# Optimization experiments

Hardware: AMD Instinct MI355X
Metric: run time of the kernel (lower is better)

The kernel has to match this reference:

```python
import jax, jax.numpy as jnp
import numpy as np

HIDDEN = 1024
HEADS = 16
HEAD_DIM = HIDDEN // HEADS


def setup_inputs() -> dict:
    key = jax.random.key(0)
    kx, kw = jax.random.split(key)
    x = jax.random.normal(kx, (1, 4096, HIDDEN), dtype=jnp.float32)
    # torch Linear weight is [out, in]; we store as [in, out] for x @ W
    W_qkv = jax.random.normal(kw, (HIDDEN, 3 * HIDDEN), dtype=jnp.float32) * (HIDDEN ** -0.5)
    return {"x": x, "W_qkv": W_qkv}


def reference(x, W_qkv):
    B, T, _ = x.shape
    qkv = x @ W_qkv                                    # [B, T, 3*HIDDEN]
    qkv = qkv.reshape(B, T, 3, HEADS, HEAD_DIM)
    qkv = jnp.transpose(qkv, (2, 0, 3, 1, 4))          # [3, B, H, T, Dh]
    q, k, v = qkv[0], qkv[1], qkv[2]
    scale = HEAD_DIM ** -0.5
    attn = jnp.einsum("bhqd,bhkd->bhqk", q, k) * scale  # [B, H, T, T] materialized (naive)
    attn = jax.nn.softmax(attn, axis=-1)
    out = jnp.einsum("bhqk,bhkd->bhqd", attn, v)        # [B, H, T, Dh]
    out = jnp.transpose(out, (0, 2, 1, 3)).reshape(B, T, HIDDEN)
    return out
```

## Files before the change

kernel.cpp:

```cpp
#include <hip/hip_runtime.h>

#define SEQ 4096
#define HID 1024
#define NH  16
#define DH  64
#define N3  3072

typedef __attribute__((ext_vector_type(4))) float floatx4;
typedef __attribute__((ext_vector_type(8))) short shortx8;
typedef __attribute__((ext_vector_type(4))) short shortx4;

__device__ __forceinline__ short f2bf(float f) {
    return (short)((__builtin_bit_cast(unsigned, f) + 0x8000u) >> 16);
}
__device__ __forceinline__ unsigned pk2bf(float a, float b) {
    unsigned ua = __builtin_bit_cast(unsigned, a) + 0x8000u;
    unsigned ub = __builtin_bit_cast(unsigned, b) + 0x8000u;
    return (ua >> 16) | (ub & 0xFFFF0000u);
}
__device__ __forceinline__ shortx4 pk4bf(float a, float b, float c, float d) {
    union { unsigned u[2]; shortx4 s; } x;
    x.u[0] = pk2bf(a, b);
    x.u[1] = pk2bf(c, d);
    return x.s;
}

#if __has_builtin(__builtin_amdgcn_exp2f)
#define fexp2 __builtin_amdgcn_exp2f
#else
#define fexp2 exp2f
#endif

#define mfma32 __builtin_amdgcn_mfma_f32_16x16x32_bf16

__device__ __forceinline__ void gll16(const short* g, short* l) {
    __builtin_amdgcn_global_load_lds(
        (const __attribute__((address_space(1))) unsigned*)g,
        (__attribute__((address_space(3))) unsigned*)l, 16, 0, 0);
}

__global__ __launch_bounds__(256) void convert_x(
    const float* __restrict__ x, short* __restrict__ Xb)
{
    size_t i = (size_t)blockIdx.x * 256 + threadIdx.x;
    float4 v = *(const float4*)&x[i * 4];
    shortx4 b = pk4bf(v.x, v.y, v.z, v.w);
    *(shortx4*)&Xb[i * 4] = b;
}

__global__ __launch_bounds__(256) void transpose_W(
    const float* __restrict__ W, short* __restrict__ Wt)
{
    __shared__ short Ws[128 * 40];
    const int t  = threadIdx.x;
    const int n0 = blockIdx.x * 128;
    const int k0 = blockIdx.y * 32;
    #pragma unroll
    for (int i = 0; i < 4; i++) {
        int idx = t + i * 256;
        int k = idx >> 5, c4 = idx & 31;
        float4 v = *(const float4*)&W[(size_t)(k0 + k) * N3 + n0 + c4 * 4];
        Ws[(c4 * 4 + 0) * 40 + k] = f2bf(v.x);
        Ws[(c4 * 4 + 1) * 40 + k] = f2bf(v.y);
        Ws[(c4 * 4 + 2) * 40 + k] = f2bf(v.z);
        Ws[(c4 * 4 + 3) * 40 + k] = f2bf(v.w);
    }
    __syncthreads();
    #pragma unroll
    for (int i = 0; i < 2; i++) {
        int idx = t + i * 256;
        int n = idx >> 2, seg = idx & 3;
        shortx8 g = *(const shortx8*)&Ws[n * 40 + seg * 8];
        *(shortx8*)&Wt[(size_t)(n0 + n) * HID + k0 + seg * 8] = g;
    }
}

#define LDC 136
__global__ __launch_bounds__(256) void qkv_gemm(
    const short* __restrict__ Xb, const short* __restrict__ Wt,
    short* __restrict__ Qb, short* __restrict__ Kb, short* __restrict__ Vb)
{
    __shared__ short SM[18432];
    short* As = SM;
    short* Bs = SM + 128 * 64;
    const int tid  = threadIdx.x;
    const int m0   = blockIdx.x * 128;
    const int n0   = blockIdx.y * 128;
    const int lane = tid & 63;
    const int wid  = tid >> 6;
    const int wm   = (wid >> 1) * 64;
    const int wn   = (wid & 1) * 64;
    const int l15  = lane & 15;
    const int quad = lane >> 4;

    floatx4 acc[4][4];
    #pragma unroll
    for (int i = 0; i < 4; i++)
        #pragma unroll
        for (int j = 0; j < 4; j++)
            acc[i][j] = (floatx4){0.f, 0.f, 0.f, 0.f};

    const int arow = tid >> 3, ac = tid & 7;
    const int swk  = (ac ^ (arow & 7)) << 3;
    const short* ag = Xb + (size_t)(m0 + arow) * HID + swk;
    const short* bg = Wt + (size_t)(n0 + arow) * HID + swk;
    short* al = As + (size_t)(tid & 192) * 8;
    short* bl = Bs + (size_t)(tid & 192) * 8;
    const int r7 = l15 & 7;

    for (int k0 = 0; k0 < HID; k0 += 64) {
        #pragma unroll
        for (int i = 0; i < 4; i++)
            gll16(ag + (size_t)i * 32 * HID + k0, al + i * 2048);
        #pragma unroll
        for (int i = 0; i < 4; i++)
            gll16(bg + (size_t)i * 32 * HID + k0, bl + i * 2048);
        __syncthreads();
        #pragma unroll
        for (int kh = 0; kh < 2; kh++) {
            shortx8 af[4], bf[4];
            #pragma unroll
            for (int t = 0; t < 4; t++) {
                int R = wm + t * 16 + l15;
                af[t] = *(const shortx8*)&As[(R << 6) + ((((kh << 2) + quad) ^ r7) << 3)];
                int Rb = wn + t * 16 + l15;
                bf[t] = *(const shortx8*)&Bs[(Rb << 6) + ((((kh << 2) + quad) ^ r7) << 3)];
            }
            #pragma unroll
            for (int tm = 0; tm < 4; tm++)
                #pragma unroll
                for (int tn = 0; tn < 4; tn++)
                    acc[tm][tn] = mfma32(af[tm], bf[tn], acc[tm][tn], 0, 0, 0);
        }
        __syncthreads();
    }

    short* Cs = SM;
    const float sc = (n0 < 1024) ? 0.18033688011112042f : 1.0f;
    #pragma unroll
    for (int tm = 0; tm < 4; tm++)
        #pragma unroll
        for (int tn = 0; tn < 4; tn++)
            #pragma unroll
            for (int r = 0; r < 4; r++)
                Cs[(wm + tm * 16 + quad * 4 + r) * LDC + wn + tn * 16 + l15] =
                    f2bf(acc[tm][tn][r] * sc);
    __syncthreads();
    short* base = (n0 < 1024) ? Qb : (n0 < 2048 ? Kb : Vb);
    const int h0 = (n0 & 1023) >> 6;
    #pragma unroll
    for (int j = 0; j < 8; j++) {
        int idx = tid + j * 256;
        int row = idx >> 4, col = (idx & 15) * 8;
        shortx8 v = *(const shortx8*)&Cs[row * LDC + col];
        *(shortx8*)&base[((size_t)(h0 + (col >> 6)) * SEQ + m0 + row) * DH + (col & 63)] = v;
    }
}

__global__ __launch_bounds__(256) void transpose_V(
    const short* __restrict__ Vb, short* __restrict__ Vt)
{
    __shared__ short Ts[64 * 72];
    const int t  = threadIdx.x;
    const int t0 = blockIdx.x * 64;
    const int h  = blockIdx.y;
    #pragma unroll
    for (int i = 0; i < 2; i++) {
        int idx = t + i * 256;
        int r = idx >> 3, seg = idx & 7;
        shortx8 g = *(const shortx8*)&Vb[((size_t)h * SEQ + t0 + r) * DH + seg * 8];
        *(shortx8*)&Ts[r * 72 + seg * 8] = g;
    }
    __syncthreads();
    #pragma unroll
    for (int i = 0; i < 2; i++) {
        int idx = t + i * 256;
        int d = idx >> 3, tseg = idx & 7;
        shortx8 g;
        #pragma unroll
        for (int j = 0; j < 8; j++) g[j] = Ts[(tseg * 8 + j) * 72 + d];
        *(shortx8*)&Vt[((size_t)h * DH + d) * SEQ + t0 + tseg * 8] = g;
    }
}

__global__ __launch_bounds__(256) void flash_attn(
    const short* __restrict__ Qb, const short* __restrict__ Kb,
    const short* __restrict__ Vt, float* __restrict__ out,
    float* __restrict__ Opart, float* __restrict__ Lpart,
    int kpc, int nit, int final)
{
    __shared__ short Ks[2][4096];
    __shared__ short Vs[2][4096];
    const int tid  = threadIdx.x;
    const int lane = tid & 63;
    const int l15  = lane & 15;
    const int quad = lane >> 4;
    const int h    = blockIdx.y;
    const int ch   = blockIdx.z;
    const int q0   = blockIdx.x * 128 + (tid >> 6) * 32;
    const int tstart = ch * kpc;
    const shortx8 ones8 = {(short)0x3F80, (short)0x3F80, (short)0x3F80, (short)0x3F80,
                           (short)0x3F80, (short)0x3F80, (short)0x3F80, (short)0x3F80};

    const short* qp = Qb + ((size_t)h * SEQ + q0 + l15) * DH;
    shortx8 qf00 = *(const shortx8*)(qp + quad * 8);
    shortx8 qf01 = *(const shortx8*)(qp + 32 + quad * 8);
    shortx8 qf10 = *(const shortx8*)(qp + 16 * DH + quad * 8);
    shortx8 qf11 = *(const shortx8*)(qp + 16 * DH + 32 + quad * 8);

    floatx4 oacc[2][4];
    #pragma unroll
    for (int s = 0; s < 2; s++)
        #pragma unroll
        for (int dn = 0; dn < 4; dn++)
            oacc[s][dn] = (floatx4){0.f, 0.f, 0.f, 0.f};
    floatx4 lacc0 = {0.f, 0.f, 0.f, 0.f}, lacc1 = {0.f, 0.f, 0.f, 0.f};

    const int rK   = tid >> 3, sK = tid & 7;
    const int key0 = 8 * ((rK >> 2) & 3) + 4 * ((rK >> 4) & 1) + (rK & 3);
    const int swo  = (sK ^ (rK & 7)) << 3;
    const short* kg = Kb + ((size_t)h * SEQ + tstart + key0) * DH + swo;
    const short* vg = Vt + ((size_t)h * DH + rK) * SEQ + tstart + swo;
    const int wslot = (tid & 192) * 8;

    gll16(kg,            &Ks[0][wslot]);
    gll16(kg + 32 * DH,  &Ks[0][wslot + 2048]);
    gll16(vg,            &Vs[0][wslot]);
    gll16(vg + 32 * SEQ, &Vs[0][wslot + 2048]);
    kg += 64 * DH;  vg += 64;

    for (int it = 0; it < nit; it++) {
        __syncthreads();
        if (it + 1 < nit) {
            int b = (it + 1) & 1;
            gll16(kg,            &Ks[b][wslot]);
            gll16(kg + 32 * DH,  &Ks[b][wslot + 2048]);
            gll16(vg,            &Vs[b][wslot]);
            gll16(vg + 32 * SEQ, &Vs[b][wslot + 2048]);
            kg += 64 * DH;  vg += 64;
        }
        const short* ks = Ks[it & 1];
        const short* vs = Vs[it & 1];

        floatx4 st0[4], st1[4];
        #pragma unroll
        for (int tn = 0; tn < 4; tn++) {
            int R = tn * 16 + l15;
            int off = (R << 6) + ((quad ^ (R & 7)) << 3);
            shortx8 kf0 = *(const shortx8*)&ks[off];
            shortx8 kf1 = *(const shortx8*)&ks[off ^ 32];
            floatx4 a0 = {0.f, 0.f, 0.f, 0.f};
            a0 = mfma32(kf0, qf00, a0, 0, 0, 0);
            a0 = mfma32(kf1, qf01, a0, 0, 0, 0);
            st0[tn] = a0;
            floatx4 a1 = {0.f, 0.f, 0.f, 0.f};
            a1 = mfma32(kf0, qf10, a1, 0, 0, 0);
            a1 = mfma32(kf1, qf11, a1, 0, 0, 0);
            st1[tn] = a1;
        }

        union { unsigned u[4]; shortx8 s; } pa00, pa01, pa10, pa11;
        #pragma unroll
        for (int half = 0; half < 2; half++) {
            int ta = half * 2, tb = half * 2 + 1;
            unsigned* d0 = half ? pa01.u : pa00.u;
            unsigned* d1 = half ? pa11.u : pa10.u;
            d0[0] = pk2bf(fexp2(st0[ta][0]), fexp2(st0[ta][1]));
            d0[1] = pk2bf(fexp2(st0[ta][2]), fexp2(st0[ta][3]));
            d0[2] = pk2bf(fexp2(st0[tb][0]), fexp2(st0[tb][1]));
            d0[3] = pk2bf(fexp2(st0[tb][2]), fexp2(st0[tb][3]));
            d1[0] = pk2bf(fexp2(st1[ta][0]), fexp2(st1[ta][1]));
            d1[1] = pk2bf(fexp2(st1[ta][2]), fexp2(st1[ta][3]));
            d1[2] = pk2bf(fexp2(st1[tb][0]), fexp2(st1[tb][1]));
            d1[3] = pk2bf(fexp2(st1[tb][2]), fexp2(st1[tb][3]));
        }

        lacc0 = mfma32(pa00.s, ones8, lacc0, 0, 0, 0);
        lacc0 = mfma32(pa01.s, ones8, lacc0, 0, 0, 0);
        lacc1 = mfma32(pa10.s, ones8, lacc1, 0, 0, 0);
        lacc1 = mfma32(pa11.s, ones8, lacc1, 0, 0, 0);

        #pragma unroll
        for (int dn = 0; dn < 4; dn++) {
            int row = dn * 16 + l15;
            int off = (row << 6) + ((quad ^ (row & 7)) << 3);
            shortx8 va = *(const shortx8*)&vs[off];
            shortx8 vb = *(const shortx8*)&vs[off ^ 32];
            oacc[0][dn] = mfma32(pa00.s, va, oacc[0][dn], 0, 0, 0);
            oacc[0][dn] = mfma32(pa01.s, vb, oacc[0][dn], 0, 0, 0);
            oacc[1][dn] = mfma32(pa10.s, va, oacc[1][dn], 0, 0, 0);
            oacc[1][dn] = mfma32(pa11.s, vb, oacc[1][dn], 0, 0, 0);
        }
    }

    if (final) {
        #pragma unroll
        for (int r = 0; r < 4; r++) {
            float rl0 = 1.0f / lacc0[r], rl1 = 1.0f / lacc1[r];
            int query = q0 + quad * 4 + r;
            float* d0 = out + (size_t)query * HID + h * DH + l15;
            float* d1 = d0 + (size_t)16 * HID;
            #pragma unroll
            for (int dn = 0; dn < 4; dn++) {
                d0[dn * 16] = oacc[0][dn][r] * rl0;
                d1[dn * 16] = oacc[1][dn][r] * rl1;
            }
        }
    } else {
        #pragma unroll
        for (int r = 0; r < 4; r++) {
            int query = q0 + quad * 4 + r;
            float* d0 = Opart + ((size_t)ch * SEQ + query) * HID + h * DH + l15;
            float* d1 = d0 + (size_t)16 * HID;
            #pragma unroll
            for (int dn = 0; dn < 4; dn++) {
                d0[dn * 16] = oacc[0][dn][r];
                d1[dn * 16] = oacc[1][dn][r];
            }
        }
        if (l15 == 0) {
            float* lp = Lpart + ((size_t)ch * NH + h) * SEQ + q0;
            #pragma unroll
            for (int r = 0; r < 4; r++) {
                lp[quad * 4 + r]      = lacc0[r];
                lp[16 + quad * 4 + r] = lacc1[r];
            }
        }
    }
}

__global__ __launch_bounds__(256) void combine(
    const float* __restrict__ Opart, const float* __restrict__ Lpart,
    float* __restrict__ out, int chn)
{
    size_t i = ((size_t)blockIdx.x * 256 + threadIdx.x) * 4;
    int q = (int)(i >> 10);
    int h = ((int)i & 1023) >> 6;
    float4 o = {0.f, 0.f, 0.f, 0.f};
    float l = 0.f;
    for (int c = 0; c < chn; c++) {
        float4 p = *(const float4*)&Opart[(size_t)c * SEQ * HID + i];
        o.x += p.x; o.y += p.y; o.z += p.z; o.w += p.w;
        l += Lpart[((size_t)c * NH + h) * SEQ + q];
    }
    float rl = 1.0f / l;
    float4 r = {o.x * rl, o.y * rl, o.z * rl, o.w * rl};
    *(float4*)&out[i] = r;
}

extern "C" void kernel_launch(void* const* d_in, const int* in_sizes, int n_in,
                              void* d_out, int out_size, void* d_ws, size_t ws_size,
                              hipStream_t stream) {
    const float* x = (const float*)d_in[0];
    const float* W = (const float*)d_in[1];
    float* out = (float*)d_out;

    short* Xb = (short*)d_ws;
    short* Wt = Xb + (size_t)SEQ * HID;
    short* Qb = Wt + (size_t)N3 * HID;
    short* Kb = Qb + (size_t)NH * SEQ * DH;
    short* Vb = Kb + (size_t)NH * SEQ * DH;
    short* Vt = Xb;
    float* Opart = (float*)(Vb + (size_t)NH * SEQ * DH);

    const size_t need = 39845888ull
                      + 4ull * SEQ * HID * 4
                      + 4ull * NH * SEQ * 4;
    const int chn = (ws_size >= need) ? 4 : 1;
    float* Lpart = Opart + (size_t)chn * SEQ * HID;
    const int kpc = SEQ / chn, nit = kpc / 64;

    convert_x  <<<dim3(SEQ * HID / 1024), 256, 0, stream>>>(x, Xb);
    transpose_W<<<dim3(N3 / 128, HID / 32), 256, 0, stream>>>(W, Wt);
    qkv_gemm   <<<dim3(SEQ / 128, N3 / 128), 256, 0, stream>>>(Xb, Wt, Qb, Kb, Vb);
    transpose_V<<<dim3(SEQ / 64, NH), 256, 0, stream>>>(Vb, Vt);
    flash_attn <<<dim3(SEQ / 128, NH, chn), 256, 0, stream>>>(
        Qb, Kb, Vt, out, Opart, Lpart, kpc, nit, chn == 1);
    if (chn > 1)
        combine<<<dim3(SEQ * HID / 1024), 256, 0, stream>>>(Opart, Lpart, out, chn);
}
```

Before: 214.5 us.

## Software-pipeline flash attention PV with next QK and swap GEMM grid order

The flash attention loop is restructured so the P·V MFMAs for the previous tile run while the current tile's QK scores are computed, and the exp/pack work is deferred. V gets a triple buffer so the tile still being consumed is not overwritten by the prefetch. A prologue and epilogue handle the first and last tiles. Separately, the QKV GEMM grid is transposed so consecutive blocks walk along N, which changes L2 reuse of the X and W tiles. The cost is more shared memory and more live registers in the attention kernel.

Measured after the change: 216.4 us. No clear change (+0.9%).

```diff
diff --git a/kernel.cpp b/kernel.cpp
--- a/kernel.cpp
+++ b/kernel.cpp
@@ -84,8 +84,8 @@
     short* As = SM;
     short* Bs = SM + 128 * 64;
     const int tid  = threadIdx.x;
-    const int m0   = blockIdx.x * 128;
-    const int n0   = blockIdx.y * 128;
+    const int n0   = blockIdx.x * 128;
+    const int m0   = blockIdx.y * 128;
     const int lane = tid & 63;
     const int wid  = tid >> 6;
     const int wm   = (wid >> 1) * 64;
@@ -190,7 +190,7 @@
     int kpc, int nit, int final)
 {
     __shared__ short Ks[2][4096];
-    __shared__ short Vs[2][4096];
+    __shared__ short Vs[3][4096];
     const int tid  = threadIdx.x;
     const int lane = tid & 63;
     const int l15  = lane & 15;
@@ -228,19 +228,67 @@
     gll16(vg,            &Vs[0][wslot]);
     gll16(vg + 32 * SEQ, &Vs[0][wslot + 2048]);
     kg += 64 * DH;  vg += 64;
-
-    for (int it = 0; it < nit; it++) {
+    __syncthreads();
+    if (nit > 1) {
+        gll16(kg,            &Ks[1][wslot]);
+        gll16(kg + 32 * DH,  &Ks[1][wslot + 2048]);
+        gll16(vg,            &Vs[1][wslot]);
+        gll16(vg + 32 * SEQ, &Vs[1][wslot + 2048]);
+        kg += 64 * DH;  vg += 64;
+    }
+
+    shortx8 pa00, pa01, pa10, pa11;
+    {
+        floatx4 st0[4], st1[4];
+        #pragma unroll
+        for (int tn = 0; tn < 4; tn++) {
+            int R = tn * 16 + l15;
+            int off = (R << 6) + ((quad ^ (R & 7)) << 3);
+            shortx8 kf0 = *(const shortx8*)&Ks[0][off];
+            shortx8 kf1 = *(const shortx8*)&Ks[0][off ^ 32];
+            floatx4 a0 = {0.f, 0.f, 0.f, 0.f};
+            a0 = mfma32(kf0, qf00, a0, 0, 0, 0);
+            a0 = mfma32(kf1, qf01, a0, 0, 0, 0);
+            st0[tn] = a0;
+            floatx4 a1 = {0.f, 0.f, 0.f, 0.f};
+            a1 = mfma32(kf0, qf10, a1, 0, 0, 0);
+            a1 = mfma32(kf1, qf11, a1, 0, 0, 0);
+            st1[tn] = a1;
+        }
+        union { unsigned u[4]; shortx8 s; } w00, w01, w10, w11;
+        #pragma unroll
+        for (int hf = 0; hf < 2; hf++) {
+            int ta = hf * 2, tb = hf * 2 + 1;
+            unsigned* d0 = hf ? w01.u : w00.u;
+            unsigned* d1 = hf ? w11.u : w10.u;
+            d0[0] = pk2bf(fexp2(st0[ta][0]), fexp2(st0[ta][1]));
+            d0[1] = pk2bf(fexp2(st0[ta][2]), fexp2(st0[ta][3]));
+            d0[2] = pk2bf(fexp2(st0[tb][0]), fexp2(st0[tb][1]));
+            d0[3] = pk2bf(fexp2(st0[tb][2]), fexp2(st0[tb][3]));
+            d1[0] = pk2bf(fexp2(st1[ta][0]), fexp2(st1[ta][1]));
+            d1[1] = pk2bf(fexp2(st1[ta][2]), fexp2(st1[ta][3]));
+            d1[2] = pk2bf(fexp2(st1[tb][0]), fexp2(st1[tb][1]));
+            d1[3] = pk2bf(fexp2(st1[tb][2]), fexp2(st1[tb][3]));
+        }
+        pa00 = w00.s; pa01 = w01.s; pa10 = w10.s; pa11 = w11.s;
+        lacc0 = mfma32(pa00, ones8, lacc0, 0, 0, 0);
+        lacc0 = mfma32(pa01, ones8, lacc0, 0, 0, 0);
+        lacc1 = mfma32(pa10, ones8, lacc1, 0, 0, 0);
+        lacc1 = mfma32(pa11, ones8, lacc1, 0, 0, 0);
+    }
+
+    int vprev = 0;
+    for (int it = 1; it < nit; it++) {
         __syncthreads();
         if (it + 1 < nit) {
-            int b = (it + 1) & 1;
-            gll16(kg,            &Ks[b][wslot]);
-            gll16(kg + 32 * DH,  &Ks[b][wslot + 2048]);
-            gll16(vg,            &Vs[b][wslot]);
-            gll16(vg + 32 * SEQ, &Vs[b][wslot + 2048]);
+            int vb = vprev + 2; if (vb >= 3) vb -= 3;
+            gll16(kg,            &Ks[(it + 1) & 1][wslot]);
+            gll16(kg + 32 * DH,  &Ks[(it + 1) & 1][wslot + 2048]);
+            gll16(vg,            &Vs[vb][wslot]);
+            gll16(vg + 32 * SEQ, &Vs[vb][wslot + 2048]);
             kg += 64 * DH;  vg += 64;
         }
         const short* ks = Ks[it & 1];
-        const short* vs = Vs[it & 1];
 
         floatx4 st0[4], st1[4];
         #pragma unroll
@@ -259,37 +307,59 @@
             st1[tn] = a1;
         }
 
-        union { unsigned u[4]; shortx8 s; } pa00, pa01, pa10, pa11;
-        #pragma unroll
-        for (int half = 0; half < 2; half++) {
-            int ta = half * 2, tb = half * 2 + 1;
-            unsigned* d0 = half ? pa01.u : pa00.u;
-            unsigned* d1 = half ? pa11.u : pa10.u;
-            d0[0] = pk2bf(fexp2(st0[ta][0]), fexp2(st0[ta][1]));
-            d0[1] = pk2bf(fexp2(st0[ta][2]), fexp2(st0[ta][3]));
-            d0[2] = pk2bf(fexp2(st0[tb][0]), fexp2(st0[tb][1]));
-            d0[3] = pk2bf(fexp2(st0[tb][2]), fexp2(st0[tb][3]));
-            d1[0] = pk2bf(fexp2(st1[ta][0]), fexp2(st1[ta][1]));
-            d1[1] = pk2bf(fexp2(st1[ta][2]), fexp2(st1[ta][3]));
-            d1[2] = pk2bf(fexp2(st1[tb][0]), fexp2(st1[tb][1]));
-            d1[3] = pk2bf(fexp2(st1[tb][2]), fexp2(st1[tb][3]));
-        }
-
-        lacc0 = mfma32(pa00.s, ones8, lacc0, 0, 0, 0);
-        lacc0 = mfma32(pa01.s, ones8, lacc0, 0, 0, 0);
-        lacc1 = mfma32(pa10.s, ones8, lacc1, 0, 0, 0);
-        lacc1 = mfma32(pa11.s, ones8, lacc1, 0, 0, 0);
-
+        {
+            const short* vs = Vs[vprev];
+            #pragma unroll
+            for (int dn = 0; dn < 4; dn++) {
+                int row = dn * 16 + l15;
+                int off = (row << 6) + ((quad ^ (row & 7)) << 3);
+                shortx8 va = *(const shortx8*)&vs[off];
+                shortx8 vb = *(const shortx8*)&vs[off ^ 32];
+                oacc[0][dn] = mfma32(pa00, va, oacc[0][dn], 0, 0, 0);
+                oacc[0][dn] = mfma32(pa01, vb, oacc[0][dn], 0, 0, 0);
+                oacc[1][dn] = mfma32(pa10, va, oacc[1][dn], 0, 0, 0);
+                oacc[1][dn] = mfma32(pa11, vb, oacc[1][dn], 0, 0, 0);
+            }
+        }
+
+        {
+            union { unsigned u[4]; shortx8 s; } w00, w01, w10, w11;
+            #pragma unroll
+            for (int hf = 0; hf < 2; hf++) {
+                int ta = hf * 2, tb = hf * 2 + 1;
+                unsigned* d0 = hf ? w01.u : w00.u;
+                unsigned* d1 = hf ? w11.u : w10.u;
+                d0[0] = pk2bf(fexp2(st0[ta][0]), fexp2(st0[ta][1]));
+                d0[1] = pk2bf(fexp2(st0[ta][2]), fexp2(st0[ta][3]));
+                d0[2] = pk2bf(fexp2(st0[tb][0]), fexp2(st0[tb][1]));
+                d0[3] = pk2bf(fexp2(st0[tb][2]), fexp2(st0[tb][3]));
+                d1[0] = pk2bf(fexp2(st1[ta][0]), fexp2(st1[ta][1]));
+                d1[1] = pk2bf(fexp2(st1[ta][2]), fexp2(st1[ta][3]));
+                d1[2] = pk2bf(fexp2(st1[tb][0]), fexp2(st1[tb][1]));
+                d1[3] = pk2bf(fexp2(st1[tb][2]), fexp2(st1[tb][3]));
+            }
+            pa00 = w00.s; pa01 = w01.s; pa10 = w10.s; pa11 = w11.s;
+        }
+        lacc0 = mfma32(pa00, ones8, lacc0, 0, 0, 0);
+        lacc0 = mfma32(pa01, ones8, lacc0, 0, 0, 0);
+        lacc1 = mfma32(pa10, ones8, lacc1, 0, 0, 0);
+        lacc1 = mfma32(pa11, ones8, lacc1, 0, 0, 0);
+
+        vprev++; if (vprev >= 3) vprev = 0;
+    }
+
+    {
+        const short* vs = Vs[vprev];
         #pragma unroll
         for (int dn = 0; dn < 4; dn++) {
             int row = dn * 16 + l15;
             int off = (row << 6) + ((quad ^ (row & 7)) << 3);
             shortx8 va = *(const shortx8*)&vs[off];
             shortx8 vb = *(const shortx8*)&vs[off ^ 32];
-            oacc[0][dn] = mfma32(pa00.s, va, oacc[0][dn], 0, 0, 0);
-            oacc[0][dn] = mfma32(pa01.s, vb, oacc[0][dn], 0, 0, 0);
-            oacc[1][dn] = mfma32(pa10.s, va, oacc[1][dn], 0, 0, 0);
-            oacc[1][dn] = mfma32(pa11.s, vb, oacc[1][dn], 0, 0, 0);
+            oacc[0][dn] = mfma32(pa00, va, oacc[0][dn], 0, 0, 0);
+            oacc[0][dn] = mfma32(pa01, vb, oacc[0][dn], 0, 0, 0);
+            oacc[1][dn] = mfma32(pa10, va, oacc[1][dn], 0, 0, 0);
+            oacc[1][dn] = mfma32(pa11, vb, oacc[1][dn], 0, 0, 0);
         }
     }
 
@@ -372,7 +442,7 @@
 
     convert_x  <<<dim3(SEQ * HID / 1024), 256, 0, stream>>>(x, Xb);
     transpose_W<<<dim3(N3 / 128, HID / 32), 256, 0, stream>>>(W, Wt);
-    qkv_gemm   <<<dim3(SEQ / 128, N3 / 128), 256, 0, stream>>>(Xb, Wt, Qb, Kb, Vb);
+    qkv_gemm   <<<dim3(N3 / 128, SEQ / 128), 256, 0, stream>>>(Xb, Wt, Qb, Kb, Vb);
     transpose_V<<<dim3(SEQ / 64, NH), 256, 0, stream>>>(Vb, Vt);
     flash_attn <<<dim3(SEQ / 128, NH, chn), 256, 0, stream>>>(
         Qb, Kb, Vt, out, Opart, Lpart, kpc, nit, chn == 1);
```
